# Kernel tuning notes

Measured on AMD Instinct MI355X. Metric: run time of the kernel, lower is better.

## Reference

```python
import jax, jax.numpy as jnp
import numpy as np


def setup_inputs() -> dict:
    key = jax.random.key(0)
    B, M, S, H, D = 1, 32768, 512, 8, 64
    ks = jax.random.split(key, 5)
    f = lambda k, shape: jax.random.normal(k, shape, dtype=jnp.float32)
    return {
        "mem_keys": f(ks[0], (B, M, H, D)),
        "mem_vals": f(ks[1], (B, M, H, D)),
        "keys": f(ks[2], (B, S, H, D)),
        "values": f(ks[3], (B, S, H, D)),
        "queries": f(ks[4], (B, S, H, D)),
        "start_of_sequence": jnp.zeros((B,), dtype=jnp.bool_),
        "write_index": 0,
    }


def reference(mem_keys, mem_vals, keys, values, queries, start_of_sequence, write_index):
    """DenseKVMemory: start_segment (clear), read (joint attention), end_segment (scatter write).

    Returns (y, new_mem_keys, new_mem_vals, new_write_index).
    """
    B, S, H, D = keys.shape
    M = mem_keys.shape[1]
    dtype = mem_keys.dtype

    # --- start_segment: clear memory at document boundaries ---
    keep = jnp.logical_not(start_of_sequence).astype(dtype).reshape(B, 1, 1, 1)
    mem_keys_c = mem_keys * keep
    mem_vals_c = mem_vals * keep

    # --- read: joint attention over [memory (no mask), segment (causal mask)] ---
    scale = float(D) ** -0.5  # default 1/sqrt(head_size) when attention_scale_factor is None
    q = queries * jnp.asarray(scale, dtype)
    mem_logits = jnp.einsum('bqhd,bkhd->bhqk', q, mem_keys_c)  # [B,H,S,M]
    seg_logits = jnp.einsum('bqhd,bkhd->bhqk', q, keys)        # [B,H,S,S]

    # kq_pos = key_pos - (query_pos + queries_offset); queries_offset = 0 at segment start.
    # causal_mask True (kq_pos < 0): key strictly before query -> allowed.
    kq_pos = jnp.arange(S)[None, :] - jnp.arange(S)[:, None]
    causal_mask = kq_pos < 0  # [S,S]
    neg_inf = jnp.asarray(jnp.finfo(dtype).min, dtype)
    seg_logits = jnp.where(causal_mask[None, None, :, :], seg_logits, neg_inf)

    all_logits = jnp.concatenate([mem_logits, seg_logits], axis=-1)  # [B,H,S,M+S]
    weights = jax.nn.softmax(all_logits, axis=-1)
    all_vals = jnp.concatenate([mem_vals_c, values], axis=1)         # [B,M+S,H,D]
    y = jnp.einsum('bhqk,bkhd->bqhd', weights, all_vals)             # [B,S,H,D]

    # --- end_segment: scatter-write segment KV into the ring buffer ---
    wi = jnp.asarray(write_index, jnp.int32)
    new_mem_keys = jax.lax.dynamic_update_slice_in_dim(mem_keys_c, keys, wi, axis=1)
    new_mem_vals = jax.lax.dynamic_update_slice_in_dim(mem_vals_c, values, wi, axis=1)
    new_write_index = (wi + S) % M
    return (y, new_mem_keys, new_mem_vals, new_write_index)
```

## Files before the change

kernel.cpp:

```cpp
#include <hip/hip_runtime.h>
#include <hip/hip_bf16.h>

typedef __bf16 bf16x8 __attribute__((ext_vector_type(8)));
typedef __bf16 bf16x4 __attribute__((ext_vector_type(4)));
typedef __bf16 bf16x2 __attribute__((ext_vector_type(2)));
typedef float f32x4 __attribute__((ext_vector_type(4)));

#define M_MEM 32768
#define S_SEG 512
#define H_ 8
#define D_ 64
#define NKEY 33280
#define NTILES 520
#define LOG2E 1.44269504088896340736f
#define CMAX (14.0f * LOG2E)

#define Y_OFF 0
#define NK_OFF 262144
#define WI_OFF (262144 + 2 * 16777216)

__global__ __launch_bounds__(256, 4) void fused_attn(
    const float* __restrict__ memk, const float* __restrict__ memv,
    const float* __restrict__ keys, const float* __restrict__ vals,
    const float* __restrict__ qry, const unsigned char* __restrict__ sos,
    const int* __restrict__ wip, float* __restrict__ out,
    float* __restrict__ opart, float* __restrict__ lst, int NC) {
  const int bid = blockIdx.x;
  const int tid = threadIdx.x;
  const int c = bid >> 6;
  const int h = (bid >> 3) & 7;
  const int qt = bid & 7;
  const int w = tid >> 6;
  const int lane = tid & 63;
  const int L = lane & 15;
  const int quad = lane >> 4;
  const float keep = sos[0] ? 0.0f : 1.0f;

  int wi_raw = wip[0];
  int wi = wi_raw < 0 ? 0 : (wi_raw > M_MEM - S_SEG ? M_MEM - S_SEG : wi_raw);
  if (bid == 0 && tid == 0) {
    int nwi = (int)(((long long)wi_raw + S_SEG) % M_MEM);
    if (nwi < 0) nwi += M_MEM;
    out[WI_OFF] = (float)nwi;
  }

  __shared__ __align__(16) __bf16 Ks[64 * 72];
  __shared__ __align__(16) __bf16 Vt[64 * 72];
  __shared__ __align__(16) __bf16 Pt[4][16 * 64];

  const int qrow_base = qt * 64 + w * 16;
  const int q_abs = qrow_base + L;

  bf16x8 qf[2];
  {
    const float* qp = qry + ((size_t)q_abs * H_ + h) * D_;
    const float qs = 0.125f * LOG2E;
#pragma unroll
    for (int kb = 0; kb < 2; ++kb) {
      const int d = kb * 32 + quad * 8;
      float4 x0 = *(const float4*)(qp + d);
      float4 x1 = *(const float4*)(qp + d + 4);
      bf16x8 f;
      f[0] = (__bf16)(x0.x * qs); f[1] = (__bf16)(x0.y * qs);
      f[2] = (__bf16)(x0.z * qs); f[3] = (__bf16)(x0.w * qs);
      f[4] = (__bf16)(x1.x * qs); f[5] = (__bf16)(x1.y * qs);
      f[6] = (__bf16)(x1.z * qs); f[7] = (__bf16)(x1.w * qs);
      qf[kb] = f;
    }
  }

  f32x4 acc[4];
#pragma unroll
  for (int g = 0; g < 4; ++g) acc[g] = (f32x4){0.f, 0.f, 0.f, 0.f};
  float l_acc = 0.f;

  const int tile_start = (NTILES * c) / NC;
  const int tile_end = (NTILES * (c + 1)) / NC;
  const int nt = tile_end - tile_start;

  const int kk = tid >> 2;
  const int d0 = (tid & 3) * 16;
  const int vp2 = tid & 31;
  const int dvb = (tid >> 5) * 8;

  float4 kreg[4], vreg[4];
  float mult;
  auto issue = [&](int t) {
    const int tb = (tile_start + t) * 64;
    const float *kb_, *vb_;
    if (tb < M_MEM) {
      kb_ = memk + (size_t)tb * 512 + h * 64;
      vb_ = memv + (size_t)tb * 512 + h * 64;
      mult = keep;
    } else {
      kb_ = keys + (size_t)(tb - M_MEM) * 512 + h * 64;
      vb_ = vals + (size_t)(tb - M_MEM) * 512 + h * 64;
      mult = 1.0f;
    }
    const float* ks = kb_ + (size_t)kk * 512 + d0;
#pragma unroll
    for (int i = 0; i < 4; ++i) kreg[i] = *(const float4*)(ks + i * 4);
    const float* vs = vb_ + (size_t)(2 * vp2) * 512 + dvb;
    vreg[0] = *(const float4*)(vs);
    vreg[1] = *(const float4*)(vs + 4);
    vreg[2] = *(const float4*)(vs + 512);
    vreg[3] = *(const float4*)(vs + 516);
  };

  issue(0);
  for (int t = 0; t < nt; ++t) {
    const int tb = (tile_start + t) * 64;
    const float mu = mult;
    {
      bf16x8 lo, hi;
      lo[0] = (__bf16)(kreg[0].x * mu); lo[1] = (__bf16)(kreg[0].y * mu);
      lo[2] = (__bf16)(kreg[0].z * mu); lo[3] = (__bf16)(kreg[0].w * mu);
      lo[4] = (__bf16)(kreg[1].x * mu); lo[5] = (__bf16)(kreg[1].y * mu);
      lo[6] = (__bf16)(kreg[1].z * mu); lo[7] = (__bf16)(kreg[1].w * mu);
      hi[0] = (__bf16)(kreg[2].x * mu); hi[1] = (__bf16)(kreg[2].y * mu);
      hi[2] = (__bf16)(kreg[2].z * mu); hi[3] = (__bf16)(kreg[2].w * mu);
      hi[4] = (__bf16)(kreg[3].x * mu); hi[5] = (__bf16)(kreg[3].y * mu);
      hi[6] = (__bf16)(kreg[3].z * mu); hi[7] = (__bf16)(kreg[3].w * mu);
      *(bf16x8*)&Ks[kk * 72 + d0] = lo;
      *(bf16x8*)&Ks[kk * 72 + d0 + 8] = hi;
      const int col = (2 * vp2 + dvb) & 63;
      float a0[8] = {vreg[0].x, vreg[0].y, vreg[0].z, vreg[0].w,
                     vreg[1].x, vreg[1].y, vreg[1].z, vreg[1].w};
      float a1[8] = {vreg[2].x, vreg[2].y, vreg[2].z, vreg[2].w,
                     vreg[3].x, vreg[3].y, vreg[3].z, vreg[3].w};
#pragma unroll
      for (int i = 0; i < 8; ++i) {
        bf16x2 pr;
        pr[0] = (__bf16)(a0[i] * mu);
        pr[1] = (__bf16)(a1[i] * mu);
        *(bf16x2*)&Vt[(dvb + i) * 72 + col] = pr;
      }
      if ((((unsigned)(tb >> 6)) & 7u) == (unsigned)qt) {
        int krow = (tb < M_MEM) ? tb + kk : wi + (tb - M_MEM) + kk;
        bool kskip = (tb < M_MEM) && (krow >= wi && krow < wi + S_SEG);
        if (!kskip) {
          float* dK = out + NK_OFF + (size_t)krow * 512 + h * 64 + d0;
#pragma unroll
          for (int i = 0; i < 4; ++i) {
            float4 vv = kreg[i];
            vv.x *= mu; vv.y *= mu; vv.z *= mu; vv.w *= mu;
            *(float4*)(dK + i * 4) = vv;
          }
        }
        int r0 = (tb < M_MEM) ? tb + 2 * vp2 : wi + (tb - M_MEM) + 2 * vp2;
#pragma unroll
        for (int pk2 = 0; pk2 < 2; ++pk2) {
          int vrow = r0 + pk2;
          bool vskip = (tb < M_MEM) && (vrow >= wi && vrow < wi + S_SEG);
          if (!vskip) {
            float* dV = out + NK_OFF + 16777216 + (size_t)vrow * 512 + h * 64 + dvb;
            float4 u0 = vreg[pk2 * 2], u1 = vreg[pk2 * 2 + 1];
            u0.x *= mu; u0.y *= mu; u0.z *= mu; u0.w *= mu;
            u1.x *= mu; u1.y *= mu; u1.z *= mu; u1.w *= mu;
            *(float4*)(dV) = u0;
            *(float4*)(dV + 4) = u1;
          }
        }
      }
    }
    __syncthreads();
    if (t + 1 < nt) issue(t + 1);

    f32x4 sg[4];
#pragma unroll
    for (int g = 0; g < 4; ++g) {
      bf16x8 klo = *(bf16x8*)&Ks[(g * 16 + L) * 72 + quad * 8];
      bf16x8 khi = *(bf16x8*)&Ks[(g * 16 + L) * 72 + 32 + quad * 8];
      f32x4 z = (f32x4){0.f, 0.f, 0.f, 0.f};
      z = __builtin_amdgcn_mfma_f32_16x16x32_bf16(klo, qf[0], z, 0, 0, 0);
      sg[g] = __builtin_amdgcn_mfma_f32_16x16x32_bf16(khi, qf[1], z, 0, 0, 0);
    }

    const int prot = 8 * (L & 7);
#pragma unroll
    for (int g = 0; g < 4; ++g) {
      bf16x4 pk;
#pragma unroll
      for (int r = 0; r < 4; ++r) {
        const int kidx = tb + g * 16 + quad * 4 + r;
        float p = __builtin_amdgcn_exp2f(sg[g][r] - CMAX);
        const bool msk = (kidx >= M_MEM) && (kidx - M_MEM >= q_abs);
        p = msk ? 0.f : p;
        l_acc += p;
        pk[r] = (__bf16)p;
      }
      *(bf16x4*)&Pt[w][L * 64 + ((g * 16 + quad * 4 + prot) & 63)] = pk;
    }

    bf16x8 pb0 = *(bf16x8*)&Pt[w][L * 64 + ((quad * 8 + prot) & 63)];
    bf16x8 pb1 = *(bf16x8*)&Pt[w][L * 64 + ((32 + quad * 8 + prot) & 63)];
#pragma unroll
    for (int g = 0; g < 4; ++g) {
      const int vrot = g * 16 + 8 * (L >> 3);
      bf16x8 v0 = *(bf16x8*)&Vt[(g * 16 + L) * 72 + ((quad * 8 + vrot) & 63)];
      bf16x8 v1 = *(bf16x8*)&Vt[(g * 16 + L) * 72 + ((32 + quad * 8 + vrot) & 63)];
      acc[g] = __builtin_amdgcn_mfma_f32_16x16x32_bf16(v0, pb0, acc[g], 0, 0, 0);
      acc[g] = __builtin_amdgcn_mfma_f32_16x16x32_bf16(v1, pb1, acc[g], 0, 0, 0);
    }
    __syncthreads();
  }

  l_acc += __shfl_xor(l_acc, 16);
  l_acc += __shfl_xor(l_acc, 32);
  const size_t row = (size_t)h * S_SEG + q_abs;
#pragma unroll
  for (int g = 0; g < 4; ++g)
    *(f32x4*)&opart[(row * NC + c) * 64 + g * 16 + quad * 4] = acc[g];
  if (quad == 0) lst[row * NC + c] = l_acc;
}

__global__ __launch_bounds__(256) void combine(
    const float* __restrict__ opart, const float* __restrict__ lst,
    float* __restrict__ y, int NC) {
  const int idx = blockIdx.x * 256 + threadIdx.x;
  const int d = idx & 63;
  const int h = (idx >> 6) & 7;
  const int q = idx >> 9;
  const size_t row = (size_t)h * S_SEG + q;
  float num = 0.f, den = 0.f;
  for (int c = 0; c < NC; ++c) {
    num += opart[(row * NC + c) * 64 + d];
    den += lst[row * NC + c];
  }
  y[idx] = num / den;
}

extern "C" void kernel_launch(void* const* d_in, const int* in_sizes, int n_in,
                              void* d_out, int out_size, void* d_ws, size_t ws_size,
                              hipStream_t stream) {
  const float* memk = (const float*)d_in[0];
  const float* memv = (const float*)d_in[1];
  const float* keys = (const float*)d_in[2];
  const float* vals = (const float*)d_in[3];
  const float* qry  = (const float*)d_in[4];
  const unsigned char* sos = (const unsigned char*)d_in[5];
  const int* wip = (const int*)d_in[6];
  float* out = (float*)d_out;

  static const int cand[] = {20, 16, 10, 8, 5, 4, 2, 1};
  int NC = 1;
  for (int i = 0; i < 8; ++i) {
    size_t need = (size_t)cand[i] *
        ((size_t)H_ * S_SEG * D_ * 4 + (size_t)H_ * S_SEG * 4);
    if (need <= ws_size) { NC = cand[i]; break; }
  }

  float* opart = (float*)d_ws;
  float* lstp = opart + (size_t)H_ * S_SEG * NC * D_;

  fused_attn<<<NC * 64, 256, 0, stream>>>(
      memk, memv, keys, vals, qry, sos, wip, out, opart, lstp, NC);

  combine<<<1024, 256, 0, stream>>>(opart, lstp, out + Y_OFF, NC);
}
```

Measured before the change: 384.7 us.

## Double-buffer KV tiles in registers and LDS, drop trailing barrier, remap blocks

The K/V staging buffers are now double-buffered in both registers and shared memory, and global loads are prefetched two tiles ahead. This removes the second __syncthreads per iteration and hides more load latency. Block indexing now puts the head in the low bits so adjacent blocks share query tiles, and the split count drops from 20 to 12 chunks. The occupancy hint falls from 4 to 3 blocks per CU to allow the larger register and LDS footprint, at the cost of fewer resident waves and fewer blocks overall.

```diff
diff --git a/kernel.cpp b/kernel.cpp
--- a/kernel.cpp
+++ b/kernel.cpp
@@ -19,7 +19,7 @@
 #define NK_OFF 262144
 #define WI_OFF (262144 + 2 * 16777216)
 
-__global__ __launch_bounds__(256, 4) void fused_attn(
+__global__ __launch_bounds__(256, 3) void fused_attn(
     const float* __restrict__ memk, const float* __restrict__ memv,
     const float* __restrict__ keys, const float* __restrict__ vals,
     const float* __restrict__ qry, const unsigned char* __restrict__ sos,
@@ -27,9 +27,9 @@
     float* __restrict__ opart, float* __restrict__ lst, int NC) {
   const int bid = blockIdx.x;
   const int tid = threadIdx.x;
+  const int h = bid & 7;
+  const int qt = (bid >> 3) & 7;
   const int c = bid >> 6;
-  const int h = (bid >> 3) & 7;
-  const int qt = bid & 7;
   const int w = tid >> 6;
   const int lane = tid & 63;
   const int L = lane & 15;
@@ -44,8 +44,8 @@
     out[WI_OFF] = (float)nwi;
   }
 
-  __shared__ __align__(16) __bf16 Ks[64 * 72];
-  __shared__ __align__(16) __bf16 Vt[64 * 72];
+  __shared__ __align__(16) __bf16 Ks[2][64 * 72];
+  __shared__ __align__(16) __bf16 Vt[2][64 * 72];
   __shared__ __align__(16) __bf16 Pt[4][16 * 64];
 
   const int qrow_base = qt * 64 + w * 16;
@@ -83,57 +83,60 @@
   const int vp2 = tid & 31;
   const int dvb = (tid >> 5) * 8;
 
-  float4 kreg[4], vreg[4];
-  float mult;
-  auto issue = [&](int t) {
+  float4 kreg[2][4], vreg[2][4];
+  float mult[2];
+  auto issue = [&](int t, int s) {
     const int tb = (tile_start + t) * 64;
     const float *kb_, *vb_;
     if (tb < M_MEM) {
       kb_ = memk + (size_t)tb * 512 + h * 64;
       vb_ = memv + (size_t)tb * 512 + h * 64;
-      mult = keep;
+      mult[s] = keep;
     } else {
       kb_ = keys + (size_t)(tb - M_MEM) * 512 + h * 64;
       vb_ = vals + (size_t)(tb - M_MEM) * 512 + h * 64;
-      mult = 1.0f;
+      mult[s] = 1.0f;
     }
     const float* ks = kb_ + (size_t)kk * 512 + d0;
 #pragma unroll
-    for (int i = 0; i < 4; ++i) kreg[i] = *(const float4*)(ks + i * 4);
+    for (int i = 0; i < 4; ++i) kreg[s][i] = *(const float4*)(ks + i * 4);
     const float* vs = vb_ + (size_t)(2 * vp2) * 512 + dvb;
-    vreg[0] = *(const float4*)(vs);
-    vreg[1] = *(const float4*)(vs + 4);
-    vreg[2] = *(const float4*)(vs + 512);
-    vreg[3] = *(const float4*)(vs + 516);
+    vreg[s][0] = *(const float4*)(vs);
+    vreg[s][1] = *(const float4*)(vs + 4);
+    vreg[s][2] = *(const float4*)(vs + 512);
+    vreg[s][3] = *(const float4*)(vs + 516);
   };
 
-  issue(0);
+  issue(0, 0);
+  if (nt > 1) issue(1, 1);
+
   for (int t = 0; t < nt; ++t) {
+    const int cur = t & 1;
     const int tb = (tile_start + t) * 64;
-    const float mu = mult;
+    const float mu = mult[cur];
     {
       bf16x8 lo, hi;
-      lo[0] = (__bf16)(kreg[0].x * mu); lo[1] = (__bf16)(kreg[0].y * mu);
-      lo[2] = (__bf16)(kreg[0].z * mu); lo[3] = (__bf16)(kreg[0].w * mu);
-      lo[4] = (__bf16)(kreg[1].x * mu); lo[5] = (__bf16)(kreg[1].y * mu);
-      lo[6] = (__bf16)(kreg[1].z * mu); lo[7] = (__bf16)(kreg[1].w * mu);
-      hi[0] = (__bf16)(kreg[2].x * mu); hi[1] = (__bf16)(kreg[2].y * mu);
-      hi[2] = (__bf16)(kreg[2].z * mu); hi[3] = (__bf16)(kreg[2].w * mu);
-      hi[4] = (__bf16)(kreg[3].x * mu); hi[5] = (__bf16)(kreg[3].y * mu);
-      hi[6] = (__bf16)(kreg[3].z * mu); hi[7] = (__bf16)(kreg[3].w * mu);
-      *(bf16x8*)&Ks[kk * 72 + d0] = lo;
-      *(bf16x8*)&Ks[kk * 72 + d0 + 8] = hi;
+      lo[0] = (__bf16)(kreg[cur][0].x * mu); lo[1] = (__bf16)(kreg[cur][0].y * mu);
+      lo[2] = (__bf16)(kreg[cur][0].z * mu); lo[3] = (__bf16)(kreg[cur][0].w * mu);
+      lo[4] = (__bf16)(kreg[cur][1].x * mu); lo[5] = (__bf16)(kreg[cur][1].y * mu);
+      lo[6] = (__bf16)(kreg[cur][1].z * mu); lo[7] = (__bf16)(kreg[cur][1].w * mu);
+      hi[0] = (__bf16)(kreg[cur][2].x * mu); hi[1] = (__bf16)(kreg[cur][2].y * mu);
+      hi[2] = (__bf16)(kreg[cur][2].z * mu); hi[3] = (__bf16)(kreg[cur][2].w * mu);
+      hi[4] = (__bf16)(kreg[cur][3].x * mu); hi[5] = (__bf16)(kreg[cur][3].y * mu);
+      hi[6] = (__bf16)(kreg[cur][3].z * mu); hi[7] = (__bf16)(kreg[cur][3].w * mu);
+      *(bf16x8*)&Ks[cur][kk * 72 + d0] = lo;
+      *(bf16x8*)&Ks[cur][kk * 72 + d0 + 8] = hi;
       const int col = (2 * vp2 + dvb) & 63;
-      float a0[8] = {vreg[0].x, vreg[0].y, vreg[0].z, vreg[0].w,
-                     vreg[1].x, vreg[1].y, vreg[1].z, vreg[1].w};
-      float a1[8] = {vreg[2].x, vreg[2].y, vreg[2].z, vreg[2].w,
-                     vreg[3].x, vreg[3].y, vreg[3].z, vreg[3].w};
+      float a0[8] = {vreg[cur][0].x, vreg[cur][0].y, vreg[cur][0].z, vreg[cur][0].w,
+                     vreg[cur][1].x, vreg[cur][1].y, vreg[cur][1].z, vreg[cur][1].w};
+      float a1[8] = {vreg[cur][2].x, vreg[cur][2].y, vreg[cur][2].z, vreg[cur][2].w,
+                     vreg[cur][3].x, vreg[cur][3].y, vreg[cur][3].z, vreg[cur][3].w};
 #pragma unroll
       for (int i = 0; i < 8; ++i) {
         bf16x2 pr;
         pr[0] = (__bf16)(a0[i] * mu);
         pr[1] = (__bf16)(a1[i] * mu);
-        *(bf16x2*)&Vt[(dvb + i) * 72 + col] = pr;
+        *(bf16x2*)&Vt[cur][(dvb + i) * 72 + col] = pr;
       }
       if ((((unsigned)(tb >> 6)) & 7u) == (unsigned)qt) {
         int krow = (tb < M_MEM) ? tb + kk : wi + (tb - M_MEM) + kk;
@@ -142,7 +145,7 @@
           float* dK = out + NK_OFF + (size_t)krow * 512 + h * 64 + d0;
 #pragma unroll
           for (int i = 0; i < 4; ++i) {
-            float4 vv = kreg[i];
+            float4 vv = kreg[cur][i];
             vv.x *= mu; vv.y *= mu; vv.z *= mu; vv.w *= mu;
             *(float4*)(dK + i * 4) = vv;
           }
@@ -154,7 +157,7 @@
           bool vskip = (tb < M_MEM) && (vrow >= wi && vrow < wi + S_SEG);
           if (!vskip) {
             float* dV = out + NK_OFF + 16777216 + (size_t)vrow * 512 + h * 64 + dvb;
-            float4 u0 = vreg[pk2 * 2], u1 = vreg[pk2 * 2 + 1];
+            float4 u0 = vreg[cur][pk2 * 2], u1 = vreg[cur][pk2 * 2 + 1];
             u0.x *= mu; u0.y *= mu; u0.z *= mu; u0.w *= mu;
             u1.x *= mu; u1.y *= mu; u1.z *= mu; u1.w *= mu;
             *(float4*)(dV) = u0;
@@ -164,13 +167,13 @@
       }
     }
     __syncthreads();
-    if (t + 1 < nt) issue(t + 1);
+    if (t + 2 < nt) issue(t + 2, cur);
 
     f32x4 sg[4];
 #pragma unroll
     for (int g = 0; g < 4; ++g) {
-      bf16x8 klo = *(bf16x8*)&Ks[(g * 16 + L) * 72 + quad * 8];
-      bf16x8 khi = *(bf16x8*)&Ks[(g * 16 + L) * 72 + 32 + quad * 8];
+      bf16x8 klo = *(bf16x8*)&Ks[cur][(g * 16 + L) * 72 + quad * 8];
+      bf16x8 khi = *(bf16x8*)&Ks[cur][(g * 16 + L) * 72 + 32 + quad * 8];
       f32x4 z = (f32x4){0.f, 0.f, 0.f, 0.f};
       z = __builtin_amdgcn_mfma_f32_16x16x32_bf16(klo, qf[0], z, 0, 0, 0);
       sg[g] = __builtin_amdgcn_mfma_f32_16x16x32_bf16(khi, qf[1], z, 0, 0, 0);
@@ -197,12 +200,11 @@
 #pragma unroll
     for (int g = 0; g < 4; ++g) {
       const int vrot = g * 16 + 8 * (L >> 3);
-      bf16x8 v0 = *(bf16x8*)&Vt[(g * 16 + L) * 72 + ((quad * 8 + vrot) & 63)];
-      bf16x8 v1 = *(bf16x8*)&Vt[(g * 16 + L) * 72 + ((32 + quad * 8 + vrot) & 63)];
+      bf16x8 v0 = *(bf16x8*)&Vt[cur][(g * 16 + L) * 72 + ((quad * 8 + vrot) & 63)];
+      bf16x8 v1 = *(bf16x8*)&Vt[cur][(g * 16 + L) * 72 + ((32 + quad * 8 + vrot) & 63)];
       acc[g] = __builtin_amdgcn_mfma_f32_16x16x32_bf16(v0, pb0, acc[g], 0, 0, 0);
       acc[g] = __builtin_amdgcn_mfma_f32_16x16x32_bf16(v1, pb1, acc[g], 0, 0, 0);
     }
-    __syncthreads();
   }
 
   l_acc += __shfl_xor(l_acc, 16);
@@ -242,9 +244,9 @@
   const int* wip = (const int*)d_in[6];
   float* out = (float*)d_out;
 
-  static const int cand[] = {20, 16, 10, 8, 5, 4, 2, 1};
+  static const int cand[] = {12, 8, 4, 2, 1};
   int NC = 1;
-  for (int i = 0; i < 8; ++i) {
+  for (int i = 0; i < 5; ++i) {
     size_t need = (size_t)cand[i] *
         ((size_t)H_ * S_SEG * D_ * 4 + (size_t)H_ * S_SEG * 4);
     if (need <= ws_size) { NC = cand[i]; break; }
```

After: 680.0 us. +76.8%, slower.
